# Kernel optimization log

Hardware: AMD Instinct MI355X
Metric: run time of the kernel (lower is better)

Reference implementation:

```python
import jax, jax.numpy as jnp
import numpy as np

TAU = 1.0
SCALE = 0.5
LN_EPS = 1e-5
NORM_EPS = 1e-12


def setup_inputs() -> dict:
    key = jax.random.key(0)
    k1, = jax.random.split(key, 1)
    N, D = 16384, 128
    x = jax.random.normal(k1, (N, D), dtype=jnp.float32)
    gamma = jnp.ones((D,), dtype=jnp.float32)
    beta = jnp.zeros((D,), dtype=jnp.float32)
    return {"x": x, "gamma": gamma, "beta": beta}


def reference(x, gamma, beta):
    # 'cn' branch: row-normalize, full pairwise cosine sim, row softmax, aggregate
    norm = jnp.sqrt(jnp.sum(x * x, axis=1, keepdims=True))
    norm_x = x / jnp.maximum(norm, NORM_EPS)          # [N, D]
    sim = jax.nn.softmax(norm_x @ norm_x.T / TAU, axis=1)  # [N, N]
    x_neg = sim @ x                                    # [N, D]
    y = (1.0 + SCALE) * x - SCALE * x_neg
    # LayerNorm over the hidden dim
    mu = jnp.mean(y, axis=-1, keepdims=True)
    var = jnp.mean((y - mu) ** 2, axis=-1, keepdims=True)
    return (y - mu) * jax.lax.rsqrt(var + LN_EPS) * gamma + beta
```

## Files before the change

### kernel.cpp

```cpp
#include <hip/hip_runtime.h>
#include <stdint.h>

#define NN 16384
#define DD 128
#define KT 64
#define QB 128
#define KSTR 144
#define VSTR 72
#define KBYTES 9216
#define VBYTES 9216

typedef float f32x16 __attribute__((ext_vector_type(16)));
typedef long long i64;

using gv = __attribute__((address_space(1))) const void;
using lv = __attribute__((address_space(3))) void;

__global__ void k_norm(const float* __restrict__ x, uint8_t* __restrict__ nx) {
  const int wave = threadIdx.x >> 6, lane = threadIdx.x & 63;
  const int row = blockIdx.x * 4 + wave;
  const float2 v = *reinterpret_cast<const float2*>(x + (size_t)row * DD + 2 * lane);
  float ss = v.x * v.x + v.y * v.y;
#pragma unroll
  for (int m = 1; m < 64; m <<= 1) ss += __shfl_xor(ss, m);
  const float rn = 1.2011224087f / fmaxf(sqrtf(ss), 1e-12f);
  const int w = __builtin_amdgcn_cvt_pk_fp8_f32(v.x * rn, v.y * rn, 0, false);
  *reinterpret_cast<uint16_t*>(nx + (size_t)row * DD + 2 * lane) = (uint16_t)w;
}

__global__ void k_transpose(const float* __restrict__ x, uint8_t* __restrict__ xT) {
  __shared__ uint16_t tile[64 * 66];
  const int n0 = blockIdx.x * 64;
  const int t = threadIdx.x;
#pragma unroll
  for (int e = 0; e < 16; ++e) {
    const int idx = e * 256 + t;
    const int r = idx >> 6, c2 = idx & 63;
    const float2 v = *reinterpret_cast<const float2*>(x + (size_t)(n0 + r) * DD + 2 * c2);
    const int w = __builtin_amdgcn_cvt_pk_fp8_f32(v.x, v.y, 0, false);
    tile[r * 66 + c2] = (uint16_t)w;
  }
  __syncthreads();
  const uint8_t* t8 = reinterpret_cast<const uint8_t*>(tile);
#pragma unroll
  for (int e = 0; e < 8; ++e) {
    const int idx = e * 256 + t;
    const int d = idx >> 4, n4 = (idx & 15) << 2;
    uint32_t w = (uint32_t)t8[(n4 + 0) * 132 + d];
    w |= (uint32_t)t8[(n4 + 1) * 132 + d] << 8;
    w |= (uint32_t)t8[(n4 + 2) * 132 + d] << 16;
    w |= (uint32_t)t8[(n4 + 3) * 132 + d] << 24;
    *reinterpret_cast<uint32_t*>(xT + (size_t)d * NN + n0 + n4) = w;
  }
}

template <int NSPLIT>
__global__ __launch_bounds__(256, 4) void k_attn(
    const uint8_t* __restrict__ nx, const uint8_t* __restrict__ xT,
    float* __restrict__ Op, float* __restrict__ Lp) {
  __shared__ alignas(16) uint8_t Kb[2][KBYTES];
  __shared__ alignas(16) uint8_t Vb[2][VBYTES];

  const int tid = threadIdx.x;
  const int wave = tid >> 6;
  const int lane = tid & 63;
  const int rl = lane & 31;
  const int hi = lane >> 5;

  const int id = blockIdx.x;
  constexpr int gs = 8 / NSPLIT;
  const int split = (id & 7) / gs;
  const int qblock = (id >> 3) * gs + (id & (gs - 1));

  constexpr int nt = (NN / KT) / NSPLIT;
  const int t0s = split * nt;
  const int qw = qblock * QB + wave * 32;

  const int sw = wave >> 1;
  const int j0 = (wave & 1) * 5;
  const int cnt = (wave & 1) ? 4 : 5;
  uint32_t soff[5];
#pragma unroll
  for (int i = 0; i < 5; ++i) {
    const int j = j0 + i;
    const int t16 = j * 64 + lane;
    if (sw == 0) {
      soff[i] = (uint32_t)((t16 / 9) * DD + (t16 % 9) * 16);
    } else {
      const int d = (2 * t16) / 9;
      const int c0 = t16 * 16 - d * VSTR;
      soff[i] = (uint32_t)(d * NN + c0 + (c0 >= 64 ? (NN - VSTR) : 0));
    }
  }

  auto stage = [&](int tt, int buf) {
    const int k0 = tt * KT;
    const uint8_t* basep = (sw == 0) ? (nx + (size_t)k0 * DD) : (xT + k0);
    uint8_t* ldsb = (sw == 0) ? &Kb[buf][0] : &Vb[buf][0];
#pragma unroll
    for (int i = 0; i < 5; ++i)
      if (i < cnt)
        __builtin_amdgcn_global_load_lds((gv*)(basep + soff[i]),
            (lv*)(ldsb + (j0 + i) * 1024), 16, 0, 0);
  };

  i64 q8[8];
#pragma unroll
  for (int dc = 0; dc < 8; ++dc)
    q8[dc] = *reinterpret_cast<const i64*>(nx + (size_t)(qw + rl) * DD + dc * 16 + 8 * hi);

  f32x16 o[4];
#pragma unroll
  for (int dt = 0; dt < 4; ++dt)
#pragma unroll
    for (int r = 0; r < 16; ++r) o[dt][r] = 0.f;
  float lsum = 0.f;

  stage(t0s, 0);

  for (int t = 0; t < nt; ++t) {
    const int buf = t & 1;
    __builtin_amdgcn_sched_barrier(0);
    asm volatile("s_waitcnt vmcnt(0)" ::: "memory");
    __builtin_amdgcn_sched_barrier(0);
    __builtin_amdgcn_s_barrier();
    __builtin_amdgcn_sched_barrier(0);
    if (t + 1 < nt) stage(t0s + t + 1, buf ^ 1);

    const uint8_t* kb = &Kb[buf][0];
    const uint8_t* vb = &Vb[buf][0];
    i64 pa[4];

#pragma unroll
    for (int kt = 0; kt < 2; ++kt) {
      const uint8_t* kbb = kb + kt * 32 * KSTR;
      f32x16 s;
#pragma unroll
      for (int r = 0; r < 16; ++r) s[r] = 0.f;
      __builtin_amdgcn_s_setprio(1);
#pragma unroll
      for (int dc = 0; dc < 8; ++dc) {
        const i64 ka = __builtin_bit_cast(i64,
            *reinterpret_cast<const uint2*>(kbb + rl * KSTR + dc * 16 + 8 * hi));
        s = __builtin_amdgcn_mfma_f32_32x32x16_fp8_fp8(ka, q8[dc], s, 0, 0, 0);
      }
      __builtin_amdgcn_s_setprio(0);
#pragma unroll
      for (int kc = 0; kc < 2; ++kc) {
        float e[8];
#pragma unroll
        for (int j = 0; j < 8; ++j) {
          float p;
          asm("v_exp_f32 %0, %1" : "=v"(p) : "v"(s[8 * kc + j]));
          e[j] = p;
          lsum += p;
        }
        uint32_t wlo = (uint32_t)__builtin_amdgcn_cvt_pk_fp8_f32(e[0], e[1], 0, false);
        wlo = (uint32_t)__builtin_amdgcn_cvt_pk_fp8_f32(e[2], e[3], (int)wlo, true);
        uint32_t whi = (uint32_t)__builtin_amdgcn_cvt_pk_fp8_f32(e[4], e[5], 0, false);
        whi = (uint32_t)__builtin_amdgcn_cvt_pk_fp8_f32(e[6], e[7], (int)whi, true);
        asm("v_permlane32_swap_b32 %0, %1" : "+v"(wlo), "+v"(whi));
        const uint2 pd = {wlo, whi};
        pa[kt * 2 + kc] = __builtin_bit_cast(i64, pd);
      }
    }

    __builtin_amdgcn_s_setprio(1);
#pragma unroll
    for (int c4 = 0; c4 < 4; ++c4) {
      const int cb = c4 * 16 + 8 * hi;
#pragma unroll
      for (int dt = 0; dt < 4; ++dt) {
        const i64 vf = __builtin_bit_cast(i64,
            *reinterpret_cast<const uint2*>(vb + (dt * 32 + rl) * VSTR + cb));
        o[dt] = __builtin_amdgcn_mfma_f32_32x32x16_fp8_fp8(pa[c4], vf, o[dt], 0, 0, 0);
      }
    }
    __builtin_amdgcn_s_setprio(0);
  }

  const float lt = lsum + __shfl_xor(lsum, 32);
  if (hi == 0) Lp[(size_t)split * NN + qw + rl] = lt;

  float* Ob = Op + (size_t)split * NN * DD;
#pragma unroll
  for (int dt = 0; dt < 4; ++dt)
#pragma unroll
    for (int r = 0; r < 16; ++r) {
      const int q = (r & 3) + 8 * (r >> 2) + 4 * hi;
      Ob[(size_t)(qw + q) * DD + dt * 32 + rl] = o[dt][r];
    }
}

__global__ void k_final(const float* __restrict__ x, const float* __restrict__ gamma,
                        const float* __restrict__ beta, const float* __restrict__ Op,
                        const float* __restrict__ Lp, float* __restrict__ out, int nsplit) {
  const int wave = threadIdx.x >> 6, lane = threadIdx.x & 63;
  const int row = blockIdx.x * 4 + wave;
  float o0 = 0.f, o1 = 0.f, lt = 0.f;
  for (int s = 0; s < nsplit; ++s) {
    const float2 v = *reinterpret_cast<const float2*>(
        Op + (size_t)s * NN * DD + (size_t)row * DD + 2 * lane);
    o0 += v.x;
    o1 += v.y;
    lt += Lp[(size_t)s * NN + row];
  }
  const float inv = 1.0f / lt;
  const float2 xv = *reinterpret_cast<const float2*>(x + (size_t)row * DD + 2 * lane);
  float y0 = 1.5f * xv.x - 0.5f * o0 * inv;
  float y1 = 1.5f * xv.y - 0.5f * o1 * inv;
  float sum = y0 + y1;
#pragma unroll
  for (int m = 1; m < 64; m <<= 1) sum += __shfl_xor(sum, m);
  const float mu = sum * (1.0f / 128.0f);
  const float d0 = y0 - mu, d1 = y1 - mu;
  float vs = d0 * d0 + d1 * d1;
#pragma unroll
  for (int m = 1; m < 64; m <<= 1) vs += __shfl_xor(vs, m);
  const float rs = rsqrtf(vs * (1.0f / 128.0f) + 1e-5f);
  const float2 g = *reinterpret_cast<const float2*>(gamma + 2 * lane);
  const float2 b = *reinterpret_cast<const float2*>(beta + 2 * lane);
  float2 ov;
  ov.x = d0 * rs * g.x + b.x;
  ov.y = d1 * rs * g.y + b.y;
  *reinterpret_cast<float2*>(out + (size_t)row * DD + 2 * lane) = ov;
}

extern "C" void kernel_launch(void* const* d_in, const int* in_sizes, int n_in,
                              void* d_out, int out_size, void* d_ws, size_t ws_size,
                              hipStream_t stream) {
  const float* x = (const float*)d_in[0];
  const float* gamma = (const float*)d_in[1];
  const float* beta = (const float*)d_in[2];
  float* out = (float*)d_out;
  char* ws = (char*)d_ws;

  uint8_t* nx = (uint8_t*)ws;
  uint8_t* xT = (uint8_t*)(ws + (size_t)NN * DD);
  const size_t base = (size_t)2 * NN * DD;
  const size_t per = (size_t)NN * DD * 4 + (size_t)NN * 4;

  int nsplit = 2;
  if (ws_size >= base + 8 * per) nsplit = 8;
  else if (ws_size >= base + 4 * per) nsplit = 4;

  float* Op = (float*)(ws + base);
  float* Lp = (float*)(ws + base + (size_t)nsplit * NN * DD * 4);

  k_norm<<<NN / 4, 256, 0, stream>>>(x, nx);
  k_transpose<<<NN / 64, 256, 0, stream>>>(x, xT);
  if (nsplit == 8)
    k_attn<8><<<dim3((NN / QB) * 8), 256, 0, stream>>>(nx, xT, Op, Lp);
  else if (nsplit == 4)
    k_attn<4><<<dim3((NN / QB) * 4), 256, 0, stream>>>(nx, xT, Op, Lp);
  else
    k_attn<2><<<dim3((NN / QB) * 2), 256, 0, stream>>>(nx, xT, Op, Lp);
  k_final<<<NN / 4, 256, 0, stream>>>(x, gamma, beta, Op, Lp, out, nsplit);
}
```

Before: 135.6 us.

## Use 32x32x64 scaled fp8 MFMA, load K from global, split keys six ways

Replaces the 32x32x16 fp8 MFMAs with the gfx950 scaled 32x32x64 f8f6f4 MFMA, so each score tile and each PV update uses fewer, larger instructions. K tiles are now read directly from global/L2 into registers instead of being staged in LDS, which halves LDS usage. The key dimension is split six ways with uneven tile counts instead of eight, giving 768 blocks, and launch bounds drop to 3 blocks per CU. The risks are global-load latency on the K path sitting inside the inner loop, and a different block-to-CU mapping that may reduce L2 reuse.

```diff
diff --git a/kernel.cpp b/kernel.cpp
--- a/kernel.cpp
+++ b/kernel.cpp
@@ -5,16 +5,24 @@
 #define DD 128
 #define KT 64
 #define QB 128
-#define KSTR 144
 #define VSTR 72
-#define KBYTES 9216
 #define VBYTES 9216
 
 typedef float f32x16 __attribute__((ext_vector_type(16)));
-typedef long long i64;
+typedef int i32x8 __attribute__((ext_vector_type(8)));
 
 using gv = __attribute__((address_space(1))) const void;
 using lv = __attribute__((address_space(3))) void;
+
+__device__ __forceinline__ i32x8 mk8(uint4 a, uint4 b) {
+  i32x8 r;
+  r[0] = a.x; r[1] = a.y; r[2] = a.z; r[3] = a.w;
+  r[4] = b.x; r[5] = b.y; r[6] = b.z; r[7] = b.w;
+  return r;
+}
+
+#define MFMA64(A, B, C) \
+  __builtin_amdgcn_mfma_scale_f32_32x32x64_f8f6f4((A), (B), (C), 0, 0, 0, 0x7F7F7F7F, 0, 0x7F7F7F7F)
 
 __global__ void k_norm(const float* __restrict__ x, uint8_t* __restrict__ nx) {
   const int wave = threadIdx.x >> 6, lane = threadIdx.x & 63;
@@ -55,10 +63,9 @@
 }
 
 template <int NSPLIT>
-__global__ __launch_bounds__(256, 4) void k_attn(
+__global__ __launch_bounds__(256, 3) void k_attn(
     const uint8_t* __restrict__ nx, const uint8_t* __restrict__ xT,
     float* __restrict__ Op, float* __restrict__ Lp) {
-  __shared__ alignas(16) uint8_t Kb[2][KBYTES];
   __shared__ alignas(16) uint8_t Vb[2][VBYTES];
 
   const int tid = threadIdx.x;
@@ -68,46 +75,43 @@
   const int hi = lane >> 5;
 
   const int id = blockIdx.x;
-  constexpr int gs = 8 / NSPLIT;
-  const int split = (id & 7) / gs;
-  const int qblock = (id >> 3) * gs + (id & (gs - 1));
-
-  constexpr int nt = (NN / KT) / NSPLIT;
-  const int t0s = split * nt;
+  const int split = id >> 7;
+  const int qblock = id & 127;
+
+  constexpr int qtn = 256 / NSPLIT;
+  constexpr int rem = 256 % NSPLIT;
+  const int nt = qtn + (split < rem ? 1 : 0);
+  const int t0s = split * qtn + (split < rem ? split : rem);
+
   const int qw = qblock * QB + wave * 32;
 
-  const int sw = wave >> 1;
-  const int j0 = (wave & 1) * 5;
-  const int cnt = (wave & 1) ? 4 : 5;
-  uint32_t soff[5];
-#pragma unroll
-  for (int i = 0; i < 5; ++i) {
+  const int j0 = 2 * wave;
+  const int cnt = (wave == 3) ? 3 : 2;
+  uint32_t soff[3];
+#pragma unroll
+  for (int i = 0; i < 3; ++i) {
     const int j = j0 + i;
     const int t16 = j * 64 + lane;
-    if (sw == 0) {
-      soff[i] = (uint32_t)((t16 / 9) * DD + (t16 % 9) * 16);
-    } else {
-      const int d = (2 * t16) / 9;
-      const int c0 = t16 * 16 - d * VSTR;
-      soff[i] = (uint32_t)(d * NN + c0 + (c0 >= 64 ? (NN - VSTR) : 0));
-    }
+    const int d = (2 * t16) / 9;
+    const int c0 = t16 * 16 - d * VSTR;
+    soff[i] = (uint32_t)(d * NN + c0 + (c0 >= 64 ? (NN - VSTR) : 0));
   }
 
   auto stage = [&](int tt, int buf) {
-    const int k0 = tt * KT;
-    const uint8_t* basep = (sw == 0) ? (nx + (size_t)k0 * DD) : (xT + k0);
-    uint8_t* ldsb = (sw == 0) ? &Kb[buf][0] : &Vb[buf][0];
-#pragma unroll
-    for (int i = 0; i < 5; ++i)
+    const uint8_t* basep = xT + tt * KT;
+#pragma unroll
+    for (int i = 0; i < 3; ++i)
       if (i < cnt)
         __builtin_amdgcn_global_load_lds((gv*)(basep + soff[i]),
-            (lv*)(ldsb + (j0 + i) * 1024), 16, 0, 0);
+            (lv*)(&Vb[buf][0] + (j0 + i) * 1024), 16, 0, 0);
   };
 
-  i64 q8[8];
-#pragma unroll
-  for (int dc = 0; dc < 8; ++dc)
-    q8[dc] = *reinterpret_cast<const i64*>(nx + (size_t)(qw + rl) * DD + dc * 16 + 8 * hi);
+  const uint8_t* qrow = nx + (size_t)(qw + rl) * DD + 32 * hi;
+  i32x8 q8[2];
+#pragma unroll
+  for (int c = 0; c < 2; ++c)
+    q8[c] = mk8(*reinterpret_cast<const uint4*>(qrow + c * 64),
+                *reinterpret_cast<const uint4*>(qrow + c * 64 + 16));
 
   f32x16 o[4];
 #pragma unroll
@@ -127,54 +131,53 @@
     __builtin_amdgcn_sched_barrier(0);
     if (t + 1 < nt) stage(t0s + t + 1, buf ^ 1);
 
-    const uint8_t* kb = &Kb[buf][0];
+    const int k0 = (t0s + t) * KT;
     const uint8_t* vb = &Vb[buf][0];
-    i64 pa[4];
-
+    const uint8_t* kgp = nx + (size_t)k0 * DD + (size_t)rl * DD + 32 * hi;
+
+    uint32_t W0[4], W1[4];
 #pragma unroll
     for (int kt = 0; kt < 2; ++kt) {
-      const uint8_t* kbb = kb + kt * 32 * KSTR;
-      f32x16 s;
-#pragma unroll
-      for (int r = 0; r < 16; ++r) s[r] = 0.f;
+      const uint8_t* kp = kgp + kt * 32 * DD;
+      const i32x8 ka0 = mk8(*reinterpret_cast<const uint4*>(kp),
+                            *reinterpret_cast<const uint4*>(kp + 16));
+      const i32x8 ka1 = mk8(*reinterpret_cast<const uint4*>(kp + 64),
+                            *reinterpret_cast<const uint4*>(kp + 80));
+      f32x16 s = {};
       __builtin_amdgcn_s_setprio(1);
-#pragma unroll
-      for (int dc = 0; dc < 8; ++dc) {
-        const i64 ka = __builtin_bit_cast(i64,
-            *reinterpret_cast<const uint2*>(kbb + rl * KSTR + dc * 16 + 8 * hi));
-        s = __builtin_amdgcn_mfma_f32_32x32x16_fp8_fp8(ka, q8[dc], s, 0, 0, 0);
+      s = MFMA64(ka0, q8[0], s);
+      s = MFMA64(ka1, q8[1], s);
+      __builtin_amdgcn_s_setprio(0);
+      float e[16];
+#pragma unroll
+      for (int r = 0; r < 16; ++r) {
+        float p;
+        asm("v_exp_f32 %0, %1" : "=v"(p) : "v"(s[r]));
+        e[r] = p;
+        lsum += p;
       }
-      __builtin_amdgcn_s_setprio(0);
-#pragma unroll
-      for (int kc = 0; kc < 2; ++kc) {
-        float e[8];
-#pragma unroll
-        for (int j = 0; j < 8; ++j) {
-          float p;
-          asm("v_exp_f32 %0, %1" : "=v"(p) : "v"(s[8 * kc + j]));
-          e[j] = p;
-          lsum += p;
-        }
-        uint32_t wlo = (uint32_t)__builtin_amdgcn_cvt_pk_fp8_f32(e[0], e[1], 0, false);
-        wlo = (uint32_t)__builtin_amdgcn_cvt_pk_fp8_f32(e[2], e[3], (int)wlo, true);
-        uint32_t whi = (uint32_t)__builtin_amdgcn_cvt_pk_fp8_f32(e[4], e[5], 0, false);
-        whi = (uint32_t)__builtin_amdgcn_cvt_pk_fp8_f32(e[6], e[7], (int)whi, true);
-        asm("v_permlane32_swap_b32 %0, %1" : "+v"(wlo), "+v"(whi));
-        const uint2 pd = {wlo, whi};
-        pa[kt * 2 + kc] = __builtin_bit_cast(i64, pd);
+      uint32_t* W = kt ? W1 : W0;
+#pragma unroll
+      for (int g = 0; g < 4; ++g) {
+        uint32_t w = (uint32_t)__builtin_amdgcn_cvt_pk_fp8_f32(e[4 * g + 0], e[4 * g + 1], 0, false);
+        w = (uint32_t)__builtin_amdgcn_cvt_pk_fp8_f32(e[4 * g + 2], e[4 * g + 3], (int)w, true);
+        W[g] = w;
       }
     }
+#pragma unroll
+    for (int g = 0; g < 4; ++g)
+      asm("v_permlane32_swap_b32 %0, %1" : "+v"(W0[g]), "+v"(W1[g]));
+    i32x8 pa;
+    pa[0] = (int)W0[0]; pa[1] = (int)W1[0]; pa[2] = (int)W0[1]; pa[3] = (int)W1[1];
+    pa[4] = (int)W0[2]; pa[5] = (int)W1[2]; pa[6] = (int)W0[3]; pa[7] = (int)W1[3];
 
     __builtin_amdgcn_s_setprio(1);
 #pragma unroll
-    for (int c4 = 0; c4 < 4; ++c4) {
-      const int cb = c4 * 16 + 8 * hi;
-#pragma unroll
-      for (int dt = 0; dt < 4; ++dt) {
-        const i64 vf = __builtin_bit_cast(i64,
-            *reinterpret_cast<const uint2*>(vb + (dt * 32 + rl) * VSTR + cb));
-        o[dt] = __builtin_amdgcn_mfma_f32_32x32x16_fp8_fp8(pa[c4], vf, o[dt], 0, 0, 0);
-      }
+    for (int dt = 0; dt < 4; ++dt) {
+      const uint8_t* vp = vb + (dt * 32 + rl) * VSTR + 32 * hi;
+      const i32x8 vf = mk8(*reinterpret_cast<const uint4*>(vp),
+                           *reinterpret_cast<const uint4*>(vp + 16));
+      o[dt] = MFMA64(pa, vf, o[dt]);
     }
     __builtin_amdgcn_s_setprio(0);
   }
@@ -241,7 +244,7 @@
   const size_t per = (size_t)NN * DD * 4 + (size_t)NN * 4;
 
   int nsplit = 2;
-  if (ws_size >= base + 8 * per) nsplit = 8;
+  if (ws_size >= base + 6 * per) nsplit = 6;
   else if (ws_size >= base + 4 * per) nsplit = 4;
 
   float* Op = (float*)(ws + base);
@@ -249,11 +252,11 @@
 
   k_norm<<<NN / 4, 256, 0, stream>>>(x, nx);
   k_transpose<<<NN / 64, 256, 0, stream>>>(x, xT);
-  if (nsplit == 8)
-    k_attn<8><<<dim3((NN / QB) * 8), 256, 0, stream>>>(nx, xT, Op, Lp);
+  if (nsplit == 6)
+    k_attn<6><<<dim3(128 * 6), 256, 0, stream>>>(nx, xT, Op, Lp);
   else if (nsplit == 4)
-    k_attn<4><<<dim3((NN / QB) * 4), 256, 0, stream>>>(nx, xT, Op, Lp);
+    k_attn<4><<<dim3(128 * 4), 256, 0, stream>>>(nx, xT, Op, Lp);
   else
-    k_attn<2><<<dim3((NN / QB) * 2), 256, 0, stream>>>(nx, xT, Op, Lp);
+    k_attn<2><<<dim3(128 * 2), 256, 0, stream>>>(nx, xT, Op, Lp);
   k_final<<<NN / 4, 256, 0, stream>>>(x, gamma, beta, Op, Lp, out, nsplit);
 }
```

After: 163.0 us. 20.2% more time.
